# Performance work log

Hardware: AMD Instinct MI355X
Metric: run time of the kernel (lower is better)

Reference implementation:

```python
import jax, jax.numpy as jnp
import numpy as np

N = 50000      # nodes
E = 640000     # edges
F_IN = 128
F_OUT = 128


def setup_inputs() -> dict:
    key = jax.random.key(0)
    k1, k2, k3, k4, k5 = jax.random.split(key, 5)
    x = jax.random.normal(k1, (N, F_IN), jnp.float32)
    # binary observation mask (torch: mask.float())
    mask = (jax.random.uniform(k2, (N, F_IN)) < 0.5).astype(jnp.float32)
    edge_index = jax.random.randint(k3, (2, E), 0, N, dtype=jnp.int32)
    W = jax.random.normal(k4, (F_OUT, F_IN), jnp.float32) / np.sqrt(F_IN)
    b = jax.random.normal(k5, (F_OUT,), jnp.float32) * 0.01
    return {"x": x, "mask": mask, "edge_index": edge_index, "W": W, "b": b}


def reference(x, mask, edge_index, W, b):
    row, col = edge_index[0], edge_index[1]

    # --- get_symmetrically_normalized_adjacency: DAD = D^-1/2 A D^-1/2 ---
    ones_e = jnp.ones((edge_index.shape[1],), x.dtype)
    deg = jax.ops.segment_sum(ones_e, col, num_segments=N)
    dinv = jnp.where(deg > 0, deg ** -0.5, 0.0)  # inf -> 0
    w = dinv[row] * dinv[col]                    # [E] normalized edge weights

    def spmm(m):  # (adj @ m)[i] = sum_{e: row_e=i} w_e * m[col_e]
        return jax.ops.segment_sum(w[:, None] * m[col], row, num_segments=N)

    # x[x.isnan()] = 0
    x = jnp.nan_to_num(x)

    # adj @ ones_like(x) == rowsum(adj) broadcast over features
    rowsum = jax.ops.segment_sum(w, row, num_segments=N)  # [N]
    numerator = rowsum[:, None] * spmm(mask * x)          # [N, F_IN]
    denominator = spmm(mask)                              # [N, F_IN]
    ratio = jnp.nan_to_num(numerator / denominator)

    return ratio @ W.T + b
```

## Files before the change

kernel.cpp:

```cpp
#include <hip/hip_runtime.h>
#include <math.h>

#define NN 50000
#define NE 640000
#define F  128
#define PACKB 12500
#define EBLKS 256
#define ECHUNK 2500
#define CAP 64
#define WPAD 136

typedef __attribute__((ext_vector_type(8))) short short8;
typedef __attribute__((ext_vector_type(4))) float floatx4;

__device__ inline unsigned f2bf_pk(float f0, float f1) {
    unsigned u0 = __float_as_uint(f0), u1 = __float_as_uint(f1);
    u0 = (u0 + 0x7fffu + ((u0 >> 16) & 1u)) >> 16;
    u1 = (u1 + 0x7fffu + ((u1 >> 16) & 1u)) >> 16;
    return (u1 << 16) | u0;
}

__device__ inline unsigned ilv4(unsigned a, unsigned b) {
    a = (a | (a << 2)) & 0x33u; a = (a | (a << 1)) & 0x55u;
    b = (b | (b << 2)) & 0x33u; b = (b | (b << 1)) & 0x55u;
    return a | (b << 1);
}

__global__ __launch_bounds__(256) void build_kernel(const float* __restrict__ x,
                                                    const float* __restrict__ mask,
                                                    const int* __restrict__ row,
                                                    const int* __restrict__ col,
                                                    unsigned* __restrict__ mx,
                                                    unsigned char* __restrict__ rec,
                                                    int* __restrict__ cnt,
                                                    int* __restrict__ deg,
                                                    unsigned short* __restrict__ srcs) {
    if (blockIdx.x < EBLKS) {
        int e0 = blockIdx.x * ECHUNK;
        for (int e = e0 + threadIdx.x; e < e0 + ECHUNK; e += 256) {
            int r = row[e], c = col[e];
            int pos = atomicAdd(&cnt[r], 1);
            if (pos < CAP) srcs[(size_t)r * CAP + pos] = (unsigned short)c;
            atomicAdd(&deg[c], 1);
        }
    } else if (blockIdx.x < EBLKS + PACKB) {
        int lane = threadIdx.x & 63;
        int n = (blockIdx.x - EBLKS) * 4 + (threadIdx.x >> 6);
        float2 xv = ((const float2*)x)[(size_t)n * 64 + lane];
        float2 mv = ((const float2*)mask)[(size_t)n * 64 + lane];
        float x0 = (xv.x != xv.x) ? 0.f : xv.x;
        float x1 = (xv.y != xv.y) ? 0.f : xv.y;
        float p0 = (mv.x != 0.f) ? x0 : 0.f;
        float p1 = (mv.y != 0.f) ? x1 : 0.f;
        mx[(size_t)n * 64 + lane] = f2bf_pk(p0, p1);
        unsigned long long b0 = __ballot(mv.x != 0.f);
        unsigned long long b1 = __ballot(mv.y != 0.f);
        if (lane < 16) {
            unsigned nib0 = (unsigned)(b0 >> (4 * lane)) & 0xFu;
            unsigned nib1 = (unsigned)(b1 >> (4 * lane)) & 0xFu;
            rec[(size_t)n * 16 + lane] = (unsigned char)ilv4(nib0, nib1);
        }
    } else {
        int t = threadIdx.x;
        if (t < 64) mx[(size_t)NN * 64 + t] = 0u;
        if (t < 4) ((unsigned*)(rec + (size_t)NN * 16))[t] = 0u;
    }
}

__global__ __launch_bounds__(256) void gather_kernel(
        const int* __restrict__ cnt, const int* __restrict__ deg,
        const unsigned short* __restrict__ srcs,
        const uint4* __restrict__ mxv, const unsigned char* __restrict__ rec,
        unsigned* __restrict__ rb) {
    int lane = threadIdx.x & 63;
    int r = blockIdx.x * 4 + (threadIdx.x >> 6);
    int l16 = lane & 15, sub = lane >> 4;
    int L = cnt[r];
    if (L > CAP - 8) L = CAP - 8;
    int dgr = deg[r];
    float dr = (dgr > 0) ? rsqrtf((float)dgr) : 0.f;
    const unsigned short* sr = srcs + (size_t)r * CAP;
    floatx4 n0 = (floatx4)(0.f), n1 = (floatx4)(0.f);
    floatx4 d0 = (floatx4)(0.f), d1 = (floatx4)(0.f);
    float S = 0.f;

    for (int j = 0; j < L; j += 8) {
        #pragma unroll
        for (int g = 0; g < 2; g++) {
            int idx = j + 4 * g + sub;
            unsigned c = sr[idx];
            c = (idx < L) ? c : (unsigned)NN;
            int dc = deg[c];
            float w = (dc > 0) ? rsqrtf((float)dc) : 0.f;
            unsigned mb = rec[(size_t)c * 16 + l16];
            uint4 u = mxv[c * 16u + l16];
            floatx4 fa, fb;
            fa.x = __uint_as_float(u.x << 16); fa.y = __uint_as_float(u.x & 0xffff0000u);
            fa.z = __uint_as_float(u.y << 16); fa.w = __uint_as_float(u.y & 0xffff0000u);
            fb.x = __uint_as_float(u.z << 16); fb.y = __uint_as_float(u.z & 0xffff0000u);
            fb.z = __uint_as_float(u.w << 16); fb.w = __uint_as_float(u.w & 0xffff0000u);
            n0 += w * fa;
            n1 += w * fb;
            d0.x += (mb & 1u) ? w : 0.f;
            d0.y += ((mb >> 1) & 1u) ? w : 0.f;
            d0.z += ((mb >> 2) & 1u) ? w : 0.f;
            d0.w += ((mb >> 3) & 1u) ? w : 0.f;
            d1.x += ((mb >> 4) & 1u) ? w : 0.f;
            d1.y += ((mb >> 5) & 1u) ? w : 0.f;
            d1.z += ((mb >> 6) & 1u) ? w : 0.f;
            d1.w += ((mb >> 7) & 1u) ? w : 0.f;
            S += w;
        }
    }

    float num[8] = {n0.x, n0.y, n0.z, n0.w, n1.x, n1.y, n1.z, n1.w};
    float den[8] = {d0.x, d0.y, d0.z, d0.w, d1.x, d1.y, d1.z, d1.w};
    #pragma unroll
    for (int q = 0; q < 8; q++) {
        num[q] += __shfl_xor(num[q], 16); num[q] += __shfl_xor(num[q], 32);
        den[q] += __shfl_xor(den[q], 16); den[q] += __shfl_xor(den[q], 32);
    }
    S += __shfl_xor(S, 16); S += __shfl_xor(S, 32);

    if (sub == 0) {
        float kf = dr * S;
        float o[8];
        #pragma unroll
        for (int q = 0; q < 8; q++)
            o[q] = (den[q] != 0.f) ? kf * num[q] / den[q] : 0.f;
        uint4 pk;
        pk.x = f2bf_pk(o[0], o[1]);
        pk.y = f2bf_pk(o[2], o[3]);
        pk.z = f2bf_pk(o[4], o[5]);
        pk.w = f2bf_pk(o[6], o[7]);
        ((uint4*)rb)[(size_t)r * 16 + l16] = pk;
    }
}

__global__ __launch_bounds__(256) void gemm_kernel(const unsigned short* __restrict__ Ab,
                                                   const float* __restrict__ W,
                                                   const float* __restrict__ bias,
                                                   float* __restrict__ out) {
    __shared__ unsigned short Wlds[F * WPAD];
    int tid = threadIdx.x;

    for (int i = tid * 4; i < F * F; i += 256 * 4) {
        int c = i >> 7, k = i & 127;
        float4 v = *(const float4*)(W + i);
        unsigned lo = f2bf_pk(v.x, v.y);
        unsigned hi = f2bf_pk(v.z, v.w);
        *(uint2*)&Wlds[c * WPAD + k] = make_uint2(lo, hi);
    }
    __syncthreads();

    int lane = tid & 63, wid = tid >> 6;
    int m = lane & 15, quad = lane >> 4;
    int arow = blockIdx.x * 64 + wid * 16 + m;
    int lrow = (arow < NN) ? arow : (NN - 1);
    const unsigned short* Arow = Ab + (size_t)lrow * F + quad * 8;

    floatx4 acc[8];
    #pragma unroll
    for (int nt = 0; nt < 8; nt++) acc[nt] = (floatx4)(0.f);

    #pragma unroll
    for (int step = 0; step < 4; step++) {
        short8 af = *(const short8*)(Arow + step * 32);
        #pragma unroll
        for (int nt = 0; nt < 8; nt++) {
            short8 bf = *(const short8*)&Wlds[(nt * 16 + m) * WPAD + step * 32 + quad * 8];
            acc[nt] = __builtin_amdgcn_mfma_f32_16x16x32_bf16(af, bf, acc[nt], 0, 0, 0);
        }
    }

    int orow0 = blockIdx.x * 64 + wid * 16 + quad * 4;
    #pragma unroll
    for (int nt = 0; nt < 8; nt++) {
        float bv = bias[nt * 16 + m];
        #pragma unroll
        for (int p = 0; p < 4; p++) {
            int gr = orow0 + p;
            if (gr < NN)
                __builtin_nontemporal_store(acc[nt][p] + bv, out + (size_t)gr * F + nt * 16 + m);
        }
    }
}

extern "C" void kernel_launch(void* const* d_in, const int* in_sizes, int n_in,
                              void* d_out, int out_size, void* d_ws, size_t ws_size,
                              hipStream_t stream) {
    const float* x    = (const float*)d_in[0];
    const float* mask = (const float*)d_in[1];
    const int*   ei   = (const int*)d_in[2];
    const float* W    = (const float*)d_in[3];
    const float* b    = (const float*)d_in[4];
    float* out = (float*)d_out;

    const int* row = ei;
    const int* col = ei + NE;

    unsigned*       mx   = (unsigned*)d_ws;
    unsigned*       rb   = mx + (size_t)(NN + 1) * 64;
    unsigned short* srcs = (unsigned short*)(rb + (size_t)NN * 64);
    int*            cnt  = (int*)(srcs + (size_t)NN * CAP);
    int*            deg  = cnt + NN;
    unsigned char*  rec  = (unsigned char*)(deg + NN + 1);

    hipMemsetAsync(cnt, 0, (size_t)(2 * NN + 1) * sizeof(int), stream);

    build_kernel<<<EBLKS + PACKB + 1, 256, 0, stream>>>(x, mask, row, col,
                                                        mx, rec, cnt, deg, srcs);
    gather_kernel<<<NN / 4, 256, 0, stream>>>(cnt, deg, srcs,
                                              (const uint4*)mx, rec, rb);
    gemm_kernel<<<(NN + 63) / 64, 256, 0, stream>>>((const unsigned short*)rb, W, b, out);
}
```

Before: 195.2 us.

## Build CSR and degrees with range-partitioned LDS atomics, precompute inverse-sqrt degree

Edge binning now uses 16 blocks of 1024 threads. Each block owns a contiguous node range, scans all edges, and counts with shared-memory atomics instead of global atomics, which also removes the memset. The per-node inverse-sqrt degree is computed once and stored next to the mask bits in a 32-byte record, so the gather reads one record instead of a degree load plus rsqrt. The cost is that every one of the 16 blocks reads the whole edge list, so only 16 CUs do the edge work and this phase could become a serial bottleneck.

```diff
diff --git a/kernel.cpp b/kernel.cpp
--- a/kernel.cpp
+++ b/kernel.cpp
@@ -4,9 +4,10 @@
 #define NN 50000
 #define NE 640000
 #define F  128
-#define PACKB 12500
-#define EBLKS 256
-#define ECHUNK 2500
+#define EB 16
+#define RANGE 3136
+#define TB 1024
+#define PACKB 3125
 #define CAP 64
 #define WPAD 136
 
@@ -26,26 +27,43 @@
     return a | (b << 1);
 }
 
-__global__ __launch_bounds__(256) void build_kernel(const float* __restrict__ x,
-                                                    const float* __restrict__ mask,
-                                                    const int* __restrict__ row,
-                                                    const int* __restrict__ col,
-                                                    unsigned* __restrict__ mx,
-                                                    unsigned char* __restrict__ rec,
-                                                    int* __restrict__ cnt,
-                                                    int* __restrict__ deg,
-                                                    unsigned short* __restrict__ srcs) {
-    if (blockIdx.x < EBLKS) {
-        int e0 = blockIdx.x * ECHUNK;
-        for (int e = e0 + threadIdx.x; e < e0 + ECHUNK; e += 256) {
+__global__ __launch_bounds__(1024) void build_kernel(const float* __restrict__ x,
+                                                     const float* __restrict__ mask,
+                                                     const int* __restrict__ row,
+                                                     const int* __restrict__ col,
+                                                     unsigned* __restrict__ mx,
+                                                     unsigned char* __restrict__ rec,
+                                                     int* __restrict__ cnt,
+                                                     unsigned short* __restrict__ srcs) {
+    if (blockIdx.x < EB) {
+        __shared__ int cl[RANGE];
+        __shared__ int dl[RANGE];
+        int t = threadIdx.x;
+        for (int i = t; i < RANGE; i += TB) { cl[i] = 0; dl[i] = 0; }
+        __syncthreads();
+        int lo = blockIdx.x * RANGE;
+        for (int e = t; e < NE; e += TB) {
             int r = row[e], c = col[e];
-            int pos = atomicAdd(&cnt[r], 1);
-            if (pos < CAP) srcs[(size_t)r * CAP + pos] = (unsigned short)c;
-            atomicAdd(&deg[c], 1);
-        }
-    } else if (blockIdx.x < EBLKS + PACKB) {
+            unsigned rr = (unsigned)(r - lo);
+            unsigned cc = (unsigned)(c - lo);
+            if (rr < RANGE) {
+                int pos = atomicAdd(&cl[rr], 1);
+                if (pos < CAP) srcs[(size_t)r * CAP + pos] = (unsigned short)c;
+            }
+            if (cc < RANGE) atomicAdd(&dl[cc], 1);
+        }
+        __syncthreads();
+        for (int i = t; i < RANGE; i += TB) {
+            int node = lo + i;
+            if (node <= NN) {
+                if (node < NN) cnt[node] = cl[i];
+                int d = dl[i];
+                *(float*)(rec + (size_t)node * 32 + 16) = (d > 0) ? rsqrtf((float)d) : 0.f;
+            }
+        }
+    } else if (blockIdx.x < EB + PACKB) {
         int lane = threadIdx.x & 63;
-        int n = (blockIdx.x - EBLKS) * 4 + (threadIdx.x >> 6);
+        int n = (blockIdx.x - EB) * 16 + (threadIdx.x >> 6);
         float2 xv = ((const float2*)x)[(size_t)n * 64 + lane];
         float2 mv = ((const float2*)mask)[(size_t)n * 64 + lane];
         float x0 = (xv.x != xv.x) ? 0.f : xv.x;
@@ -58,17 +76,17 @@
         if (lane < 16) {
             unsigned nib0 = (unsigned)(b0 >> (4 * lane)) & 0xFu;
             unsigned nib1 = (unsigned)(b1 >> (4 * lane)) & 0xFu;
-            rec[(size_t)n * 16 + lane] = (unsigned char)ilv4(nib0, nib1);
+            rec[(size_t)n * 32 + lane] = (unsigned char)ilv4(nib0, nib1);
         }
     } else {
         int t = threadIdx.x;
         if (t < 64) mx[(size_t)NN * 64 + t] = 0u;
-        if (t < 4) ((unsigned*)(rec + (size_t)NN * 16))[t] = 0u;
+        if (t < 4) ((unsigned*)(rec + (size_t)NN * 32))[t] = 0u;
     }
 }
 
 __global__ __launch_bounds__(256) void gather_kernel(
-        const int* __restrict__ cnt, const int* __restrict__ deg,
+        const int* __restrict__ cnt,
         const unsigned short* __restrict__ srcs,
         const uint4* __restrict__ mxv, const unsigned char* __restrict__ rec,
         unsigned* __restrict__ rb) {
@@ -77,8 +95,7 @@
     int l16 = lane & 15, sub = lane >> 4;
     int L = cnt[r];
     if (L > CAP - 8) L = CAP - 8;
-    int dgr = deg[r];
-    float dr = (dgr > 0) ? rsqrtf((float)dgr) : 0.f;
+    float dr = *(const float*)(rec + (size_t)r * 32 + 16);
     const unsigned short* sr = srcs + (size_t)r * CAP;
     floatx4 n0 = (floatx4)(0.f), n1 = (floatx4)(0.f);
     floatx4 d0 = (floatx4)(0.f), d1 = (floatx4)(0.f);
@@ -90,9 +107,8 @@
             int idx = j + 4 * g + sub;
             unsigned c = sr[idx];
             c = (idx < L) ? c : (unsigned)NN;
-            int dc = deg[c];
-            float w = (dc > 0) ? rsqrtf((float)dc) : 0.f;
-            unsigned mb = rec[(size_t)c * 16 + l16];
+            float w = *(const float*)(rec + (size_t)c * 32 + 16);
+            unsigned mb = rec[(size_t)c * 32 + l16];
             uint4 u = mxv[c * 16u + l16];
             floatx4 fa, fb;
             fa.x = __uint_as_float(u.x << 16); fa.y = __uint_as_float(u.x & 0xffff0000u);
@@ -203,14 +219,12 @@
     unsigned*       rb   = mx + (size_t)(NN + 1) * 64;
     unsigned short* srcs = (unsigned short*)(rb + (size_t)NN * 64);
     int*            cnt  = (int*)(srcs + (size_t)NN * CAP);
-    int*            deg  = cnt + NN;
-    unsigned char*  rec  = (unsigned char*)(deg + NN + 1);
-
-    hipMemsetAsync(cnt, 0, (size_t)(2 * NN + 1) * sizeof(int), stream);
-
-    build_kernel<<<EBLKS + PACKB + 1, 256, 0, stream>>>(x, mask, row, col,
-                                                        mx, rec, cnt, deg, srcs);
-    gather_kernel<<<NN / 4, 256, 0, stream>>>(cnt, deg, srcs,
+    unsigned char*  rec  = (unsigned char*)(cnt + NN);
+
+
+    build_kernel<<<EB + PACKB + 1, TB, 0, stream>>>(x, mask, row, col,
+                                                    mx, rec, cnt, srcs);
+    gather_kernel<<<NN / 4, 256, 0, stream>>>(cnt, srcs,
                                               (const uint4*)mx, rec, rb);
     gemm_kernel<<<(NN + 63) / 64, 256, 0, stream>>>((const unsigned short*)rb, W, b, out);
 }
```

New measurement: 563.3 us. 2.89x slower.
